# Optimization experiments

Measured on AMD Instinct MI355X. Metric: run time of the kernel, lower is better.

The kernel has to match this reference:

```python
import jax, jax.numpy as jnp
import numpy as np

B, T, I, H, CODE = 256, 512, 1, 1024, 3


def _gru_cell(x, h, Wih, Whh, bih, bhh):
    # x: [B, I], h: [B, H]; torch nn.GRU gate math
    gi = x @ Wih.T + bih            # [B, 3H]
    gh = h @ Whh.T + bhh            # [B, 3H]
    i_r, i_z, i_n = jnp.split(gi, 3, axis=-1)
    h_r, h_z, h_n = jnp.split(gh, 3, axis=-1)
    r = jax.nn.sigmoid(i_r + h_r)
    z = jax.nn.sigmoid(i_z + h_z)
    n = jnp.tanh(i_n + r * h_n)
    return (1.0 - z) * n + z * h


def setup_inputs() -> dict:
    key = jax.random.key(0)
    ks = jax.random.split(key, 16)
    s_i = 1.0 / np.sqrt(H)
    u = lambda k, shape, s: jax.random.uniform(k, shape, jnp.float32, -s, s)
    inp = {
        "input": jax.random.normal(ks[0], (B, T, I), jnp.float32),
        "hidden_state": jnp.zeros((B, H), jnp.float32),
        # encoder GRU
        "Wih_e": u(ks[1], (3 * H, I), s_i), "Whh_e": u(ks[2], (3 * H, H), s_i),
        "bih_e": u(ks[3], (3 * H,), s_i), "bhh_e": u(ks[4], (3 * H,), s_i),
        # linear_enc: H -> 3
        "Wenc": u(ks[5], (CODE, H), s_i), "benc": u(ks[6], (CODE,), s_i),
        # linear_dec: 3 -> H
        "Wdec": u(ks[7], (H, CODE), 1.0 / np.sqrt(CODE)), "bdec": u(ks[8], (H,), 1.0 / np.sqrt(CODE)),
        # decoder GRU
        "Wih_d": u(ks[9], (3 * H, I), s_i), "Whh_d": u(ks[10], (3 * H, H), s_i),
        "bih_d": u(ks[11], (3 * H,), s_i), "bhh_d": u(ks[12], (3 * H,), s_i),
        # linear_out: H -> I
        "Wout": u(ks[13], (I, H), s_i), "bout": u(ks[14], (I,), s_i),
    }
    return inp


def reference(input, hidden_state, Wih_e, Whh_e, bih_e, bhh_e,
              Wenc, benc, Wdec, bdec, Wih_d, Whh_d, bih_d, bhh_d, Wout, bout):
    # ---- Encoder: GRU over the sequence, keep final hidden state ----
    xs = jnp.swapaxes(input, 0, 1)  # [T, B, I]

    def enc_step(h, x_t):
        h = _gru_cell(x_t, h, Wih_e, Whh_e, bih_e, bhh_e)
        return h, None

    h_T, _ = jax.lax.scan(enc_step, hidden_state, xs)
    # bottleneck: linear H->3 + sigmoid (use_linear, use_activation)
    features = jax.nn.sigmoid(h_T @ Wenc.T + benc)  # [B, 3]

    h0 = features @ Wdec.T + bdec                   # [B, H]
    x0 = jnp.zeros((input.shape[0], I), input.dtype)

    def dec_step(carry, _):
        x, h = carry
        h = _gru_cell(x, h, Wih_d, Whh_d, bih_d, bhh_d)
        x = h @ Wout.T + bout                       # [B, I]
        return (x, h), x

    _, ys = jax.lax.scan(dec_step, (x0, h0), None, length=T)  # [T, B, I]
    output = jnp.swapaxes(ys, 0, 1)                 # [B, T, I]

    # ---- Masked MSE (mask is all ones in the source -> plain mean) ----
    loss = jnp.mean((input - output) ** 2)
    return loss, features, output
```

## Files before the change

kernel.cpp:

```cpp
#include <hip/hip_runtime.h>
#include <math.h>

#define B 256
#define T 512
#define H 1024
#define NBLK 256

typedef _Float16 f16x8 __attribute__((ext_vector_type(8)));
typedef float f32x4 __attribute__((ext_vector_type(4)));
typedef unsigned u32x4 __attribute__((ext_vector_type(4)));

__device__ __forceinline__ float sigmoidf_(float x) { return 1.0f / (1.0f + __expf(-x)); }
__device__ __forceinline__ float tanhf_(float x) {
    float ax = fabsf(x);
    float t = __expf(-2.0f * ax);
    float r = (1.0f - t) / (1.0f + t);
    return x < 0.f ? -r : r;
}

__device__ __forceinline__ void store_b128_coh(void* p, u32x4 v) {
    asm volatile("global_store_dwordx4 %0, %1, off sc0 sc1" :: "v"(p), "v"(v) : "memory");
}
__device__ __forceinline__ u32x4 load_b16_coh(const void* p) {
    u32x4 v;
    asm volatile("global_load_dwordx4 %0, %1, off sc0 sc1" : "=v"(v) : "v"(p));
    return v;
}
__device__ __forceinline__ void storef_coh(float* p, float v) {
    __hip_atomic_store(p, v, __ATOMIC_RELAXED, __HIP_MEMORY_SCOPE_AGENT);
}
__device__ __forceinline__ float loadf_coh(const float* p) {
    return __hip_atomic_load((float*)p, __ATOMIC_RELAXED, __HIP_MEMORY_SCOPE_AGENT);
}

__device__ __forceinline__ void load_weights(f16x8 (&wB)[48], const float* __restrict__ W,
                                             int j, int kh, int kg) {
#pragma unroll
    for (int g = 0; g < 3; ++g)
#pragma unroll
        for (int i = 0; i < 16; ++i) {
            const float* p = W + (((size_t)g << 10) + j) * 1024 + (kh << 9) + (i << 5) + (kg << 3);
            float4 u = *(const float4*)p;
            float4 v = *(const float4*)(p + 4);
            f16x8 o;
            o[0] = (_Float16)u.x; o[1] = (_Float16)u.y; o[2] = (_Float16)u.z; o[3] = (_Float16)u.w;
            o[4] = (_Float16)v.x; o[5] = (_Float16)v.y; o[6] = (_Float16)v.z; o[7] = (_Float16)v.w;
            wB[g * 16 + i] = o;
        }
}

#define PUBLISH_SYNC(hn_expr, EXTRA_STORES)                                              \
    do {                                                                                 \
        if (tid < 64) {                                                                  \
            _Float16* hn_ = (hn_expr);                                                   \
            int ch0 = tid, ch1 = tid + 64;                                               \
            store_b128_coh(hn_ + ((size_t)(b0 + (ch0 >> 3)) << 10) + j0 + (ch0 & 7) * 8, \
                           *(const u32x4*)&hout[ch0 >> 3][(ch0 & 7) * 8]);               \
            store_b128_coh(hn_ + ((size_t)(b0 + (ch1 >> 3)) << 10) + j0 + (ch1 & 7) * 8, \
                           *(const u32x4*)&hout[ch1 >> 3][(ch1 & 7) * 8]);               \
        }                                                                                \
        EXTRA_STORES                                                                     \
        if (tid >= 128 && tid < 144) {                                                   \
            unsigned tgt = gcur + 1;                                                     \
            while (__hip_atomic_load(&tags[(bt * 16 + (tid - 128)) * 32],                \
                                     __ATOMIC_RELAXED, __HIP_MEMORY_SCOPE_AGENT) < tgt)  \
                __builtin_amdgcn_s_sleep(1);                                             \
        }                                                                                \
        if (tid < 64) {                                                                  \
            asm volatile("s_waitcnt vmcnt(0)" ::: "memory");                             \
            if (tid == 0)                                                                \
                __hip_atomic_store(&tags[(bt * 16 + jt) * 32], gcur + 1,                 \
                                   __ATOMIC_RELAXED, __HIP_MEMORY_SCOPE_AGENT);          \
        }                                                                                \
        __syncthreads();                                                                 \
        ++gcur;                                                                          \
    } while (0)

template <bool DEC>
__device__ __forceinline__ void run_phase(
    int b0, int j0, int bt, int jt, int j, int np, int kh, int kg, int r16,
    int tid, int lane,
    const f16x8 (&wB)[48], float (&hreg)[4],
    _Float16* __restrict__ h16A, _Float16* __restrict__ h16B,
    const float* __restrict__ Wih, const float* __restrict__ bih,
    const float* __restrict__ bhh,
    const float* __restrict__ input, const float* __restrict__ Wout, float bout_v,
    float* __restrict__ xpart, float* __restrict__ outp,
    unsigned* tags, unsigned& gcur,
    char* Als, f32x4 (*red)[3][64], _Float16 (*hout)[64], float* xv_s, float (*xnp)[16])
{
    const float wi_r = Wih[j], wi_z = Wih[H + j], wi_n = Wih[2 * H + j];
    const float bi_r = bih[j], bi_z = bih[H + j], bi_n = bih[2 * H + j];
    const float bh_r = bhh[j], bh_z = bhh[H + j], bh_n = bhh[2 * H + j];
    const float wo = DEC ? Wout[j] : 0.f;
    const int kc = tid & 127, rb = tid >> 7;

    for (int t = 0; t < T; ++t) {
        const _Float16* hp = (t & 1) ? h16B : h16A;
        _Float16* hn = (t & 1) ? h16A : h16B;

        u32x4 tmp[4];
#pragma unroll
        for (int i = 0; i < 4; ++i) {
            int row = i * 4 + rb;
            tmp[i] = load_b16_coh(hp + ((size_t)(b0 + row) << 10) + (kc << 3));
        }
        float xg = 0.f;
        if (DEC && t > 0 && tid < 16) {
            const float* xp = xpart + ((t - 1) & 1) * 4096 + (size_t)(b0 + tid) * 16;
#pragma unroll
            for (int q = 0; q < 16; ++q) xg += loadf_coh(xp + q);
            xg += bout_v;
        }
        asm volatile("s_waitcnt vmcnt(0)" ::: "memory");
        if (DEC && tid < 16) {
            float xv = (t > 0) ? xg : 0.f;
            xv_s[tid] = xv;
            if (t > 0 && jt == 0) outp[(size_t)(b0 + tid) * T + (t - 1)] = xv;
        }
#pragma unroll
        for (int i = 0; i < 4; ++i) {
            int row = i * 4 + rb;
            *(u32x4*)(Als + row * 2048 + ((kc << 4) ^ ((row & 7) << 4))) = tmp[i];
        }
        __syncthreads();

        f32x4 aR = {0.f, 0.f, 0.f, 0.f}, aZ = {0.f, 0.f, 0.f, 0.f}, aN = {0.f, 0.f, 0.f, 0.f};
#pragma unroll
        for (int i = 0; i < 16; ++i) {
            int kb = (kh << 10) + (i << 6) + (kg << 4);
            f16x8 a = *(const f16x8*)(Als + (r16 << 11) + (kb ^ ((r16 & 7) << 4)));
            aR = __builtin_amdgcn_mfma_f32_16x16x32_f16(a, wB[i], aR, 0, 0, 0);
            aZ = __builtin_amdgcn_mfma_f32_16x16x32_f16(a, wB[16 + i], aZ, 0, 0, 0);
            aN = __builtin_amdgcn_mfma_f32_16x16x32_f16(a, wB[32 + i], aN, 0, 0, 0);
        }
        if (kh == 1) {
            red[np][0][lane] = aR; red[np][1][lane] = aZ; red[np][2][lane] = aN;
        }
        __syncthreads();

        if (kh == 0) {
            f32x4 rR = red[np][0][lane], rZ = red[np][1][lane], rN = red[np][2][lane];
#pragma unroll
            for (int reg = 0; reg < 4; ++reg) {
                int row = kg * 4 + reg;
                int b = b0 + row;
                float xv = DEC ? xv_s[row] : input[(size_t)b * T + t];
                float r = sigmoidf_(xv * wi_r + bi_r + aR[reg] + rR[reg] + bh_r);
                float z = sigmoidf_(xv * wi_z + bi_z + aZ[reg] + rZ[reg] + bh_z);
                float n = tanhf_(xv * wi_n + bi_n + r * (aN[reg] + rN[reg] + bh_n));
                float hNew = (1.f - z) * n + z * hreg[reg];
                hreg[reg] = hNew;
                hout[row][np * 16 + r16] = (_Float16)hNew;
                if (DEC) {
                    float v = hNew * wo;
                    v += __shfl_xor(v, 1); v += __shfl_xor(v, 2);
                    v += __shfl_xor(v, 4); v += __shfl_xor(v, 8);
                    if (r16 == 0) xnp[np][row] = v;
                }
            }
        }
        __syncthreads();

        PUBLISH_SYNC(hn,
            if (DEC && tid < 16) {
                float s_ = xnp[0][tid] + xnp[1][tid] + xnp[2][tid] + xnp[3][tid];
                storef_coh(xpart + (t & 1) * 4096 + (size_t)(b0 + tid) * 16 + jt, s_);
            }
        );
    }
}

__global__ __launch_bounds__(512, 2) void gru_persistent(
    const float* __restrict__ input, const float* __restrict__ h_init,
    const float* __restrict__ Wih_e, const float* __restrict__ Whh_e,
    const float* __restrict__ bih_e, const float* __restrict__ bhh_e,
    const float* __restrict__ Wenc, const float* __restrict__ benc,
    const float* __restrict__ Wdec, const float* __restrict__ bdec,
    const float* __restrict__ Wih_d, const float* __restrict__ Whh_d,
    const float* __restrict__ bih_d, const float* __restrict__ bhh_d,
    const float* __restrict__ Wout, const float* __restrict__ boutp,
    float* __restrict__ featOut, float* __restrict__ outp,
    _Float16* __restrict__ h16A, _Float16* __restrict__ h16B,
    float* __restrict__ xpart, float* __restrict__ fpart,
    unsigned* tags)
{
    __shared__ __align__(16) char Als[32768];
    __shared__ f32x4 red[4][3][64];
    __shared__ __align__(16) _Float16 hout[16][64];
    __shared__ float xv_s[16];
    __shared__ float xnp[4][16];
    __shared__ float fp_np[4][16][3];
    __shared__ float feats[16][3];

    const int tid = threadIdx.x;
    const int lane = tid & 63;
    const int wv = tid >> 6;
    const int kh = wv & 1;
    const int np = wv >> 1;
    const int kg = lane >> 4;
    const int r16 = lane & 15;
    const int bid = blockIdx.x;
    const int bt = bid & 15, jt = bid >> 4;
    const int b0 = bt * 16, j0 = jt * 64;
    const int j = j0 + np * 16 + r16;
    const float bout_v = boutp[0];
    unsigned gcur = 0;

    f16x8 wB[48];
    float hreg[4] = {0.f, 0.f, 0.f, 0.f};

    if (kh == 0) {
#pragma unroll
        for (int reg = 0; reg < 4; ++reg) {
            int row = kg * 4 + reg;
            float v = h_init[((size_t)(b0 + row) << 10) + j];
            hreg[reg] = v;
            hout[row][np * 16 + r16] = (_Float16)v;
        }
    }
    __syncthreads();
    PUBLISH_SYNC(h16A, );
    load_weights(wB, Whh_e, j, kh, kg);

    run_phase<false>(b0, j0, bt, jt, j, np, kh, kg, r16, tid, lane, wB, hreg,
                     h16A, h16B, Wih_e, bih_e, bhh_e, input, Wout, bout_v,
                     xpart, outp, tags, gcur, Als, red, hout, xv_s, xnp);

    {
        float we0 = Wenc[j], we1 = Wenc[H + j], we2 = Wenc[2 * H + j];
        if (kh == 0) {
#pragma unroll
            for (int reg = 0; reg < 4; ++reg) {
                float h = hreg[reg];
                float q0 = h * we0, q1 = h * we1, q2 = h * we2;
#pragma unroll
                for (int m = 1; m < 16; m <<= 1) {
                    q0 += __shfl_xor(q0, m);
                    q1 += __shfl_xor(q1, m);
                    q2 += __shfl_xor(q2, m);
                }
                if (r16 == 0) {
                    fp_np[np][kg * 4 + reg][0] = q0;
                    fp_np[np][kg * 4 + reg][1] = q1;
                    fp_np[np][kg * 4 + reg][2] = q2;
                }
            }
        }
        __syncthreads();
        if (tid < 48) {
            int bi = tid / 3, c = tid % 3;
            float s = fp_np[0][bi][c] + fp_np[1][bi][c] + fp_np[2][bi][c] + fp_np[3][bi][c];
            storef_coh(fpart + (size_t)(b0 + bi) * 48 + jt * 3 + c, s);
        }
        if (tid >= 128 && tid < 144) {
            unsigned tgt = gcur + 1;
            while (__hip_atomic_load(&tags[(bt * 16 + (tid - 128)) * 32],
                                     __ATOMIC_RELAXED, __HIP_MEMORY_SCOPE_AGENT) < tgt)
                __builtin_amdgcn_s_sleep(1);
        }
        if (tid < 64) {
            asm volatile("s_waitcnt vmcnt(0)" ::: "memory");
            if (tid == 0)
                __hip_atomic_store(&tags[(bt * 16 + jt) * 32], gcur + 1,
                                   __ATOMIC_RELAXED, __HIP_MEMORY_SCOPE_AGENT);
        }
        __syncthreads();
        ++gcur;

        if (tid < 48) {
            int bi = tid / 3, c = tid % 3;
            float s = 0.f;
            const float* fp = fpart + (size_t)(b0 + bi) * 48 + c;
#pragma unroll
            for (int q = 0; q < 16; ++q) s += loadf_coh(fp + q * 3);
            float f = sigmoidf_(s + benc[c]);
            feats[bi][c] = f;
            if (jt == 0) featOut[(b0 + bi) * 3 + c] = f;
        }
        __syncthreads();

        if (kh == 0) {
#pragma unroll
            for (int reg = 0; reg < 4; ++reg) {
                int row = kg * 4 + reg;
                float v = feats[row][0] * Wdec[j * 3 + 0] + feats[row][1] * Wdec[j * 3 + 1] +
                          feats[row][2] * Wdec[j * 3 + 2] + bdec[j];
                hreg[reg] = v;
                hout[row][np * 16 + r16] = (_Float16)v;
            }
        }
        __syncthreads();
        PUBLISH_SYNC(h16A, );
        load_weights(wB, Whh_d, j, kh, kg);
    }

    run_phase<true>(b0, j0, bt, jt, j, np, kh, kg, r16, tid, lane, wB, hreg,
                    h16A, h16B, Wih_d, bih_d, bhh_d, input, Wout, bout_v,
                    xpart, outp, tags, gcur, Als, red, hout, xv_s, xnp);

    if (jt == 0 && tid < 16) {
        const float* xp = xpart + 4096 + (size_t)(b0 + tid) * 16;
        float s = 0.f;
#pragma unroll
        for (int q = 0; q < 16; ++q) s += loadf_coh(xp + q);
        outp[(size_t)(b0 + tid) * T + (T - 1)] = s + bout_v;
    }
}

__global__ __launch_bounds__(256) void loss_partial(
    const float* __restrict__ input, const float* __restrict__ outp,
    float* __restrict__ partial)
{
    int idx = blockIdx.x * blockDim.x + threadIdx.x;
    float s = 0.f;
    for (int i = idx; i < B * T; i += gridDim.x * blockDim.x) {
        float d = input[i] - outp[i];
        s += d * d;
    }
#pragma unroll
    for (int off = 32; off; off >>= 1) s += __shfl_down(s, off);
    __shared__ float ws[4];
    if ((threadIdx.x & 63) == 0) ws[threadIdx.x >> 6] = s;
    __syncthreads();
    if (threadIdx.x == 0) partial[blockIdx.x] = ws[0] + ws[1] + ws[2] + ws[3];
}

__global__ __launch_bounds__(256) void loss_final(
    const float* __restrict__ partial, float* __restrict__ loss)
{
    int tid = threadIdx.x;
    float s = partial[tid];
#pragma unroll
    for (int off = 32; off; off >>= 1) s += __shfl_down(s, off);
    __shared__ float ws[4];
    if ((tid & 63) == 0) ws[tid >> 6] = s;
    __syncthreads();
    if (tid == 0) loss[0] = (ws[0] + ws[1] + ws[2] + ws[3]) * (1.0f / (float)(B * T));
}

extern "C" void kernel_launch(void* const* d_in, const int* in_sizes, int n_in,
                              void* d_out, int out_size, void* d_ws, size_t ws_size,
                              hipStream_t stream) {
    const float* input = (const float*)d_in[0];
    const float* h_init = (const float*)d_in[1];
    const float* Wih_e = (const float*)d_in[2];
    const float* Whh_e = (const float*)d_in[3];
    const float* bih_e = (const float*)d_in[4];
    const float* bhh_e = (const float*)d_in[5];
    const float* Wenc  = (const float*)d_in[6];
    const float* benc  = (const float*)d_in[7];
    const float* Wdec  = (const float*)d_in[8];
    const float* bdec  = (const float*)d_in[9];
    const float* Wih_d = (const float*)d_in[10];
    const float* Whh_d = (const float*)d_in[11];
    const float* bih_d = (const float*)d_in[12];
    const float* bhh_d = (const float*)d_in[13];
    const float* Wout  = (const float*)d_in[14];
    const float* bout  = (const float*)d_in[15];
    (void)in_sizes; (void)n_in; (void)out_size; (void)ws_size;

    float* out = (float*)d_out;
    float* lossp = out;
    float* feat = out + 1;
    float* outp = out + 1 + B * 3;

    char* ws = (char*)d_ws;
    _Float16* h16A = (_Float16*)ws;                  ws += (size_t)B * H * 2;
    _Float16* h16B = (_Float16*)ws;                  ws += (size_t)B * H * 2;
    float* xpart = (float*)ws;                       ws += 2 * 4096 * 4;
    float* fpart = (float*)ws;                       ws += (size_t)B * 48 * 4;
    float* partial = (float*)ws;                     ws += 256 * 4;
    unsigned* tags = (unsigned*)ws;                  ws += 16 * 16 * 32 * 4;

    hipMemsetAsync(tags, 0, 16 * 16 * 32 * 4, stream);

    gru_persistent<<<dim3(NBLK), dim3(512), 0, stream>>>(
        input, h_init, Wih_e, Whh_e, bih_e, bhh_e, Wenc, benc, Wdec, bdec,
        Wih_d, Whh_d, bih_d, bhh_d, Wout, bout,
        feat, outp, h16A, h16B, xpart, fpart, tags);

    loss_partial<<<256, 256, 0, stream>>>(input, outp, partial);
    loss_final<<<1, 256, 0, stream>>>(partial, lossp);
}
```

Before: 5.966 ms.

## Publish hidden state per wave with per-stripe tags instead of block barriers

Each kh==0 wave now writes its own 16-column stripe of the new hidden state and raises a per-wave tag. A single waiter wave polls all 64 stripe tags at the start of the next step, which removes the block-wide publish barrier and the extra __syncthreads at the end of every step. The decoder's output partial sums are written directly per wave into a wider xpart buffer and then reduced with vector loads and shuffles, dropping the shared xnp stage. This shortens the serial critical path of the recurrence at the cost of more tags to poll and more global partials to read.

```diff
diff --git a/kernel.cpp b/kernel.cpp
--- a/kernel.cpp
+++ b/kernel.cpp
@@ -26,11 +26,22 @@
     asm volatile("global_load_dwordx4 %0, %1, off sc0 sc1" : "=v"(v) : "v"(p));
     return v;
 }
+__device__ __forceinline__ f32x4 load_f128_coh(const void* p) {
+    f32x4 v;
+    asm volatile("global_load_dwordx4 %0, %1, off sc0 sc1" : "=v"(v) : "v"(p));
+    return v;
+}
 __device__ __forceinline__ void storef_coh(float* p, float v) {
     __hip_atomic_store(p, v, __ATOMIC_RELAXED, __HIP_MEMORY_SCOPE_AGENT);
 }
 __device__ __forceinline__ float loadf_coh(const float* p) {
     return __hip_atomic_load((float*)p, __ATOMIC_RELAXED, __HIP_MEMORY_SCOPE_AGENT);
+}
+__device__ __forceinline__ unsigned load_tag(const unsigned* p) {
+    return __hip_atomic_load((unsigned*)p, __ATOMIC_RELAXED, __HIP_MEMORY_SCOPE_AGENT);
+}
+__device__ __forceinline__ void store_tag(unsigned* p, unsigned v) {
+    __hip_atomic_store(p, v, __ATOMIC_RELAXED, __HIP_MEMORY_SCOPE_AGENT);
 }
 
 __device__ __forceinline__ void load_weights(f16x8 (&wB)[48], const float* __restrict__ W,
@@ -49,45 +60,31 @@
         }
 }
 
-#define PUBLISH_SYNC(hn_expr, EXTRA_STORES)                                              \
+#define PUBLISH_STRIPE(HN, G)                                                            \
     do {                                                                                 \
-        if (tid < 64) {                                                                  \
-            _Float16* hn_ = (hn_expr);                                                   \
-            int ch0 = tid, ch1 = tid + 64;                                               \
-            store_b128_coh(hn_ + ((size_t)(b0 + (ch0 >> 3)) << 10) + j0 + (ch0 & 7) * 8, \
-                           *(const u32x4*)&hout[ch0 >> 3][(ch0 & 7) * 8]);               \
-            store_b128_coh(hn_ + ((size_t)(b0 + (ch1 >> 3)) << 10) + j0 + (ch1 & 7) * 8, \
-                           *(const u32x4*)&hout[ch1 >> 3][(ch1 & 7) * 8]);               \
+        if (lane < 32) {                                                                 \
+            int prow = lane >> 1, pch = lane & 1;                                        \
+            u32x4 pv = *(const u32x4*)((const char*)&hout[0][0] +                        \
+                                       prow * 128 + np * 32 + pch * 16);                 \
+            store_b128_coh((HN) + ((size_t)(b0 + prow) << 10) + j0 + np * 16 + pch * 8,  \
+                           pv);                                                          \
         }                                                                                \
-        EXTRA_STORES                                                                     \
-        if (tid >= 128 && tid < 144) {                                                   \
-            unsigned tgt = gcur + 1;                                                     \
-            while (__hip_atomic_load(&tags[(bt * 16 + (tid - 128)) * 32],                \
-                                     __ATOMIC_RELAXED, __HIP_MEMORY_SCOPE_AGENT) < tgt)  \
-                __builtin_amdgcn_s_sleep(1);                                             \
-        }                                                                                \
-        if (tid < 64) {                                                                  \
-            asm volatile("s_waitcnt vmcnt(0)" ::: "memory");                             \
-            if (tid == 0)                                                                \
-                __hip_atomic_store(&tags[(bt * 16 + jt) * 32], gcur + 1,                 \
-                                   __ATOMIC_RELAXED, __HIP_MEMORY_SCOPE_AGENT);          \
-        }                                                                                \
-        __syncthreads();                                                                 \
-        ++gcur;                                                                          \
+        asm volatile("s_waitcnt vmcnt(0)" ::: "memory");                                 \
+        if (lane == 0) store_tag(gtags + (jt * 4 + np) * 16, (G));                       \
     } while (0)
 
 template <bool DEC>
 __device__ __forceinline__ void run_phase(
     int b0, int j0, int bt, int jt, int j, int np, int kh, int kg, int r16,
-    int tid, int lane,
+    int tid, int lane, int wv,
     const f16x8 (&wB)[48], float (&hreg)[4],
     _Float16* __restrict__ h16A, _Float16* __restrict__ h16B,
     const float* __restrict__ Wih, const float* __restrict__ bih,
     const float* __restrict__ bhh,
     const float* __restrict__ input, const float* __restrict__ Wout, float bout_v,
     float* __restrict__ xpart, float* __restrict__ outp,
-    unsigned* tags, unsigned& gcur,
-    char* Als, f32x4 (*red)[3][64], _Float16 (*hout)[64], float* xv_s, float (*xnp)[16])
+    unsigned* gtags, unsigned& gcur,
+    char* Als, f32x4 (*red)[3][64], _Float16 (*hout)[64], float* xv_s)
 {
     const float wi_r = Wih[j], wi_z = Wih[H + j], wi_n = Wih[2 * H + j];
     const float bi_r = bih[j], bi_z = bih[H + j], bi_n = bih[2 * H + j];
@@ -99,24 +96,40 @@
         const _Float16* hp = (t & 1) ? h16B : h16A;
         _Float16* hn = (t & 1) ? h16A : h16B;
 
+        if (wv == 1) {
+            while (load_tag(gtags + lane * 16) < gcur) __builtin_amdgcn_s_sleep(1);
+        }
+        __builtin_amdgcn_sched_barrier(0);
+        __syncthreads();
+
         u32x4 tmp[4];
 #pragma unroll
         for (int i = 0; i < 4; ++i) {
             int row = i * 4 + rb;
             tmp[i] = load_b16_coh(hp + ((size_t)(b0 + row) << 10) + (kc << 3));
         }
-        float xg = 0.f;
-        if (DEC && t > 0 && tid < 16) {
-            const float* xp = xpart + ((t - 1) & 1) * 4096 + (size_t)(b0 + tid) * 16;
-#pragma unroll
-            for (int q = 0; q < 16; ++q) xg += loadf_coh(xp + q);
-            xg += bout_v;
+        f32x4 x0 = {0.f, 0.f, 0.f, 0.f}, x1 = x0, x2 = x0, x3 = x0;
+        if (DEC && wv == 0 && t > 0) {
+            const float* xp = xpart + ((t - 1) & 1) * 16384 +
+                              (size_t)(b0 + (lane >> 2)) * 64 + (lane & 3) * 16;
+            x0 = load_f128_coh(xp);
+            x1 = load_f128_coh(xp + 4);
+            x2 = load_f128_coh(xp + 8);
+            x3 = load_f128_coh(xp + 12);
         }
         asm volatile("s_waitcnt vmcnt(0)" ::: "memory");
-        if (DEC && tid < 16) {
-            float xv = (t > 0) ? xg : 0.f;
-            xv_s[tid] = xv;
-            if (t > 0 && jt == 0) outp[(size_t)(b0 + tid) * T + (t - 1)] = xv;
+        __builtin_amdgcn_sched_barrier(0);
+        if (DEC && wv == 0) {
+            float s = x0[0] + x0[1] + x0[2] + x0[3] + x1[0] + x1[1] + x1[2] + x1[3] +
+                      x2[0] + x2[1] + x2[2] + x2[3] + x3[0] + x3[1] + x3[2] + x3[3];
+            s += __shfl_xor(s, 1);
+            s += __shfl_xor(s, 2);
+            if ((lane & 3) == 0) {
+                int row = lane >> 2;
+                float xv = (t > 0) ? (s + bout_v) : 0.f;
+                xv_s[row] = xv;
+                if (t > 0 && jt == 0) outp[(size_t)(b0 + row) * T + (t - 1)] = xv;
+            }
         }
 #pragma unroll
         for (int i = 0; i < 4; ++i) {
@@ -156,18 +169,13 @@
                     float v = hNew * wo;
                     v += __shfl_xor(v, 1); v += __shfl_xor(v, 2);
                     v += __shfl_xor(v, 4); v += __shfl_xor(v, 8);
-                    if (r16 == 0) xnp[np][row] = v;
+                    if (r16 == 0)
+                        storef_coh(xpart + (t & 1) * 16384 + (size_t)b * 64 + jt * 4 + np, v);
                 }
             }
-        }
-        __syncthreads();
-
-        PUBLISH_SYNC(hn,
-            if (DEC && tid < 16) {
-                float s_ = xnp[0][tid] + xnp[1][tid] + xnp[2][tid] + xnp[3][tid];
-                storef_coh(xpart + (t & 1) * 4096 + (size_t)(b0 + tid) * 16 + jt, s_);
-            }
-        );
+            PUBLISH_STRIPE(hn, gcur + 1);
+        }
+        ++gcur;
     }
 }
 
@@ -189,7 +197,6 @@
     __shared__ f32x4 red[4][3][64];
     __shared__ __align__(16) _Float16 hout[16][64];
     __shared__ float xv_s[16];
-    __shared__ float xnp[4][16];
     __shared__ float fp_np[4][16][3];
     __shared__ float feats[16][3];
 
@@ -205,6 +212,7 @@
     const int b0 = bt * 16, j0 = jt * 64;
     const int j = j0 + np * 16 + r16;
     const float bout_v = boutp[0];
+    unsigned* gtags = tags + (size_t)bt * 1024;
     unsigned gcur = 0;
 
     f16x8 wB[48];
@@ -218,14 +226,14 @@
             hreg[reg] = v;
             hout[row][np * 16 + r16] = (_Float16)v;
         }
-    }
-    __syncthreads();
-    PUBLISH_SYNC(h16A, );
+        PUBLISH_STRIPE(h16A, 1u);
+    }
+    gcur = 1;
     load_weights(wB, Whh_e, j, kh, kg);
 
-    run_phase<false>(b0, j0, bt, jt, j, np, kh, kg, r16, tid, lane, wB, hreg,
+    run_phase<false>(b0, j0, bt, jt, j, np, kh, kg, r16, tid, lane, wv, wB, hreg,
                      h16A, h16B, Wih_e, bih_e, bhh_e, input, Wout, bout_v,
-                     xpart, outp, tags, gcur, Als, red, hout, xv_s, xnp);
+                     xpart, outp, gtags, gcur, Als, red, hout, xv_s);
 
     {
         float we0 = Wenc[j], we1 = Wenc[H + j], we2 = Wenc[2 * H + j];
@@ -253,20 +261,15 @@
             float s = fp_np[0][bi][c] + fp_np[1][bi][c] + fp_np[2][bi][c] + fp_np[3][bi][c];
             storef_coh(fpart + (size_t)(b0 + bi) * 48 + jt * 3 + c, s);
         }
-        if (tid >= 128 && tid < 144) {
-            unsigned tgt = gcur + 1;
-            while (__hip_atomic_load(&tags[(bt * 16 + (tid - 128)) * 32],
-                                     __ATOMIC_RELAXED, __HIP_MEMORY_SCOPE_AGENT) < tgt)
-                __builtin_amdgcn_s_sleep(1);
-        }
-        if (tid < 64) {
+        if (wv == 0) {
             asm volatile("s_waitcnt vmcnt(0)" ::: "memory");
-            if (tid == 0)
-                __hip_atomic_store(&tags[(bt * 16 + jt) * 32], gcur + 1,
-                                   __ATOMIC_RELAXED, __HIP_MEMORY_SCOPE_AGENT);
-        }
-        __syncthreads();
-        ++gcur;
+            if (lane < 4) store_tag(gtags + (jt * 4 + lane) * 16, gcur + 1);
+        }
+        if (wv == 1) {
+            while (load_tag(gtags + lane * 16) < gcur + 1) __builtin_amdgcn_s_sleep(1);
+        }
+        __builtin_amdgcn_sched_barrier(0);
+        __syncthreads();
 
         if (tid < 48) {
             int bi = tid / 3, c = tid % 3;
@@ -289,22 +292,36 @@
                 hreg[reg] = v;
                 hout[row][np * 16 + r16] = (_Float16)v;
             }
-        }
-        __syncthreads();
-        PUBLISH_SYNC(h16A, );
-        load_weights(wB, Whh_d, j, kh, kg);
-    }
-
-    run_phase<true>(b0, j0, bt, jt, j, np, kh, kg, r16, tid, lane, wB, hreg,
+            PUBLISH_STRIPE(h16A, gcur + 2);
+        }
+        gcur += 2;
+    }
+    load_weights(wB, Whh_d, j, kh, kg);
+
+    run_phase<true>(b0, j0, bt, jt, j, np, kh, kg, r16, tid, lane, wv, wB, hreg,
                     h16A, h16B, Wih_d, bih_d, bhh_d, input, Wout, bout_v,
-                    xpart, outp, tags, gcur, Als, red, hout, xv_s, xnp);
-
-    if (jt == 0 && tid < 16) {
-        const float* xp = xpart + 4096 + (size_t)(b0 + tid) * 16;
-        float s = 0.f;
-#pragma unroll
-        for (int q = 0; q < 16; ++q) s += loadf_coh(xp + q);
-        outp[(size_t)(b0 + tid) * T + (T - 1)] = s + bout_v;
+                    xpart, outp, gtags, gcur, Als, red, hout, xv_s);
+
+    if (wv == 1) {
+        while (load_tag(gtags + lane * 16) < gcur) __builtin_amdgcn_s_sleep(1);
+    }
+    __builtin_amdgcn_sched_barrier(0);
+    __syncthreads();
+    if (jt == 0 && wv == 0) {
+        const float* xp = xpart + 16384 +
+                          (size_t)(b0 + (lane >> 2)) * 64 + (lane & 3) * 16;
+        f32x4 x0 = load_f128_coh(xp);
+        f32x4 x1 = load_f128_coh(xp + 4);
+        f32x4 x2 = load_f128_coh(xp + 8);
+        f32x4 x3 = load_f128_coh(xp + 12);
+        asm volatile("s_waitcnt vmcnt(0)" ::: "memory");
+        __builtin_amdgcn_sched_barrier(0);
+        float s = x0[0] + x0[1] + x0[2] + x0[3] + x1[0] + x1[1] + x1[2] + x1[3] +
+                  x2[0] + x2[1] + x2[2] + x2[3] + x3[0] + x3[1] + x3[2] + x3[3];
+        s += __shfl_xor(s, 1);
+        s += __shfl_xor(s, 2);
+        if ((lane & 3) == 0)
+            outp[(size_t)(b0 + (lane >> 2)) * T + (T - 1)] = s + bout_v;
     }
 }
 
@@ -368,12 +385,13 @@
     char* ws = (char*)d_ws;
     _Float16* h16A = (_Float16*)ws;                  ws += (size_t)B * H * 2;
     _Float16* h16B = (_Float16*)ws;                  ws += (size_t)B * H * 2;
-    float* xpart = (float*)ws;                       ws += 2 * 4096 * 4;
+    float* xpart = (float*)ws;                       ws += 2 * 16384 * 4;
     float* fpart = (float*)ws;                       ws += (size_t)B * 48 * 4;
     float* partial = (float*)ws;                     ws += 256 * 4;
-    unsigned* tags = (unsigned*)ws;                  ws += 16 * 16 * 32 * 4;
-
-    hipMemsetAsync(tags, 0, 16 * 16 * 32 * 4, stream);
+    ws = (char*)(((uintptr_t)ws + 127) & ~(uintptr_t)127);
+    unsigned* tags = (unsigned*)ws;                  ws += 16 * 1024 * 4;
+
+    hipMemsetAsync(tags, 0, 16 * 1024 * 4, stream);
 
     gru_persistent<<<dim3(NBLK), dim3(512), 0, stream>>>(
         input, h_init, Wih_e, Whh_e, bih_e, bhh_e, Wenc, benc, Wdec, bdec,
```

Result: slower. 7.197 ms (+20.6%).

## Halve persistent grid to 128 blocks of 1024 threads, widening hidden tile

Applied to the files above, without the earlier changes.

Changes the persistent GRU decomposition from 256 blocks of 512 threads (16 batch x 64 hidden columns) to 128 blocks of 1024 threads (16 batch x 128 hidden columns). Each step's global-memory barrier now spans 8 peer blocks instead of 16, which cuts polling and tag traffic, and per-block partial-sum buffers shrink to match. In exchange each block does twice the MFMA work per step, uses more shared memory, and only half the CUs are used, so per-step compute latency may grow.

```diff
diff --git a/kernel.cpp b/kernel.cpp
--- a/kernel.cpp
+++ b/kernel.cpp
@@ -4,7 +4,7 @@
 #define B 256
 #define T 512
 #define H 1024
-#define NBLK 256
+#define NBLK 128
 
 typedef _Float16 f16x8 __attribute__((ext_vector_type(8)));
 typedef float f32x4 __attribute__((ext_vector_type(4)));
@@ -53,23 +53,25 @@
     do {                                                                                 \
         if (tid < 64) {                                                                  \
             _Float16* hn_ = (hn_expr);                                                   \
-            int ch0 = tid, ch1 = tid + 64;                                               \
-            store_b128_coh(hn_ + ((size_t)(b0 + (ch0 >> 3)) << 10) + j0 + (ch0 & 7) * 8, \
-                           *(const u32x4*)&hout[ch0 >> 3][(ch0 & 7) * 8]);               \
-            store_b128_coh(hn_ + ((size_t)(b0 + (ch1 >> 3)) << 10) + j0 + (ch1 & 7) * 8, \
-                           *(const u32x4*)&hout[ch1 >> 3][(ch1 & 7) * 8]);               \
+            _Pragma("unroll")                                                            \
+            for (int pi = 0; pi < 4; ++pi) {                                             \
+                int c = tid + 64 * pi;                                                   \
+                int prow = c >> 4, pch = c & 15;                                         \
+                store_b128_coh(hn_ + ((size_t)(b0 + prow) << 10) + j0 + pch * 8,         \
+                               *(const u32x4*)&hout[prow][pch * 8]);                     \
+            }                                                                            \
         }                                                                                \
         EXTRA_STORES                                                                     \
-        if (tid >= 128 && tid < 144) {                                                   \
+        if (tid >= 128 && tid < 136) {                                                   \
             unsigned tgt = gcur + 1;                                                     \
-            while (__hip_atomic_load(&tags[(bt * 16 + (tid - 128)) * 32],                \
+            while (__hip_atomic_load(&tags[(bt * 8 + (tid - 128)) * 32],                 \
                                      __ATOMIC_RELAXED, __HIP_MEMORY_SCOPE_AGENT) < tgt)  \
                 __builtin_amdgcn_s_sleep(1);                                             \
         }                                                                                \
         if (tid < 64) {                                                                  \
             asm volatile("s_waitcnt vmcnt(0)" ::: "memory");                             \
             if (tid == 0)                                                                \
-                __hip_atomic_store(&tags[(bt * 16 + jt) * 32], gcur + 1,                 \
+                __hip_atomic_store(&tags[(bt * 8 + jt) * 32], gcur + 1,                  \
                                    __ATOMIC_RELAXED, __HIP_MEMORY_SCOPE_AGENT);          \
         }                                                                                \
         __syncthreads();                                                                 \
@@ -87,7 +89,7 @@
     const float* __restrict__ input, const float* __restrict__ Wout, float bout_v,
     float* __restrict__ xpart, float* __restrict__ outp,
     unsigned* tags, unsigned& gcur,
-    char* Als, f32x4 (*red)[3][64], _Float16 (*hout)[64], float* xv_s, float (*xnp)[16])
+    char* Als, f32x4 (*red)[3][64], _Float16 (*hout)[128], float* xv_s, float (*xnp)[16])
 {
     const float wi_r = Wih[j], wi_z = Wih[H + j], wi_n = Wih[2 * H + j];
     const float bi_r = bih[j], bi_z = bih[H + j], bi_n = bih[2 * H + j];
@@ -99,30 +101,24 @@
         const _Float16* hp = (t & 1) ? h16B : h16A;
         _Float16* hn = (t & 1) ? h16A : h16B;
 
-        u32x4 tmp[4];
-#pragma unroll
-        for (int i = 0; i < 4; ++i) {
-            int row = i * 4 + rb;
-            tmp[i] = load_b16_coh(hp + ((size_t)(b0 + row) << 10) + (kc << 3));
-        }
+        u32x4 tmp0 = load_b16_coh(hp + ((size_t)(b0 + rb) << 10) + (kc << 3));
+        u32x4 tmp1 = load_b16_coh(hp + ((size_t)(b0 + rb + 8) << 10) + (kc << 3));
         float xg = 0.f;
         if (DEC && t > 0 && tid < 16) {
-            const float* xp = xpart + ((t - 1) & 1) * 4096 + (size_t)(b0 + tid) * 16;
-#pragma unroll
-            for (int q = 0; q < 16; ++q) xg += loadf_coh(xp + q);
+            const float* xp = xpart + ((t - 1) & 1) * 2048 + (size_t)(b0 + tid) * 8;
+#pragma unroll
+            for (int q = 0; q < 8; ++q) xg += loadf_coh(xp + q);
             xg += bout_v;
         }
         asm volatile("s_waitcnt vmcnt(0)" ::: "memory");
+        __builtin_amdgcn_sched_barrier(0);
         if (DEC && tid < 16) {
             float xv = (t > 0) ? xg : 0.f;
             xv_s[tid] = xv;
             if (t > 0 && jt == 0) outp[(size_t)(b0 + tid) * T + (t - 1)] = xv;
         }
-#pragma unroll
-        for (int i = 0; i < 4; ++i) {
-            int row = i * 4 + rb;
-            *(u32x4*)(Als + row * 2048 + ((kc << 4) ^ ((row & 7) << 4))) = tmp[i];
-        }
+        *(u32x4*)(Als + rb * 2048 + ((kc << 4) ^ ((rb & 7) << 4))) = tmp0;
+        *(u32x4*)(Als + (rb + 8) * 2048 + ((kc << 4) ^ ((rb & 7) << 4))) = tmp1;
         __syncthreads();
 
         f32x4 aR = {0.f, 0.f, 0.f, 0.f}, aZ = {0.f, 0.f, 0.f, 0.f}, aN = {0.f, 0.f, 0.f, 0.f};
@@ -164,14 +160,15 @@
 
         PUBLISH_SYNC(hn,
             if (DEC && tid < 16) {
-                float s_ = xnp[0][tid] + xnp[1][tid] + xnp[2][tid] + xnp[3][tid];
-                storef_coh(xpart + (t & 1) * 4096 + (size_t)(b0 + tid) * 16 + jt, s_);
+                float s_ = xnp[0][tid] + xnp[1][tid] + xnp[2][tid] + xnp[3][tid] +
+                           xnp[4][tid] + xnp[5][tid] + xnp[6][tid] + xnp[7][tid];
+                storef_coh(xpart + (t & 1) * 2048 + (size_t)(b0 + tid) * 8 + jt, s_);
             }
         );
     }
 }
 
-__global__ __launch_bounds__(512, 2) void gru_persistent(
+__global__ __launch_bounds__(1024) void gru_persistent(
     const float* __restrict__ input, const float* __restrict__ h_init,
     const float* __restrict__ Wih_e, const float* __restrict__ Whh_e,
     const float* __restrict__ bih_e, const float* __restrict__ bhh_e,
@@ -186,11 +183,11 @@
     unsigned* tags)
 {
     __shared__ __align__(16) char Als[32768];
-    __shared__ f32x4 red[4][3][64];
-    __shared__ __align__(16) _Float16 hout[16][64];
+    __shared__ f32x4 red[8][3][64];
+    __shared__ __align__(16) _Float16 hout[16][128];
     __shared__ float xv_s[16];
-    __shared__ float xnp[4][16];
-    __shared__ float fp_np[4][16][3];
+    __shared__ float xnp[8][16];
+    __shared__ float fp_np[8][16][3];
     __shared__ float feats[16][3];
 
     const int tid = threadIdx.x;
@@ -202,7 +199,7 @@
     const int r16 = lane & 15;
     const int bid = blockIdx.x;
     const int bt = bid & 15, jt = bid >> 4;
-    const int b0 = bt * 16, j0 = jt * 64;
+    const int b0 = bt * 16, j0 = jt * 128;
     const int j = j0 + np * 16 + r16;
     const float bout_v = boutp[0];
     unsigned gcur = 0;
@@ -250,19 +247,21 @@
         __syncthreads();
         if (tid < 48) {
             int bi = tid / 3, c = tid % 3;
-            float s = fp_np[0][bi][c] + fp_np[1][bi][c] + fp_np[2][bi][c] + fp_np[3][bi][c];
-            storef_coh(fpart + (size_t)(b0 + bi) * 48 + jt * 3 + c, s);
-        }
-        if (tid >= 128 && tid < 144) {
+            float s = 0.f;
+#pragma unroll
+            for (int q = 0; q < 8; ++q) s += fp_np[q][bi][c];
+            storef_coh(fpart + (size_t)(b0 + bi) * 24 + jt * 3 + c, s);
+        }
+        if (tid >= 128 && tid < 136) {
             unsigned tgt = gcur + 1;
-            while (__hip_atomic_load(&tags[(bt * 16 + (tid - 128)) * 32],
+            while (__hip_atomic_load(&tags[(bt * 8 + (tid - 128)) * 32],
                                      __ATOMIC_RELAXED, __HIP_MEMORY_SCOPE_AGENT) < tgt)
                 __builtin_amdgcn_s_sleep(1);
         }
         if (tid < 64) {
             asm volatile("s_waitcnt vmcnt(0)" ::: "memory");
             if (tid == 0)
-                __hip_atomic_store(&tags[(bt * 16 + jt) * 32], gcur + 1,
+                __hip_atomic_store(&tags[(bt * 8 + jt) * 32], gcur + 1,
                                    __ATOMIC_RELAXED, __HIP_MEMORY_SCOPE_AGENT);
         }
         __syncthreads();
@@ -271,9 +270,9 @@
         if (tid < 48) {
             int bi = tid / 3, c = tid % 3;
             float s = 0.f;
-            const float* fp = fpart + (size_t)(b0 + bi) * 48 + c;
-#pragma unroll
-            for (int q = 0; q < 16; ++q) s += loadf_coh(fp + q * 3);
+            const float* fp = fpart + (size_t)(b0 + bi) * 24 + c;
+#pragma unroll
+            for (int q = 0; q < 8; ++q) s += loadf_coh(fp + q * 3);
             float f = sigmoidf_(s + benc[c]);
             feats[bi][c] = f;
             if (jt == 0) featOut[(b0 + bi) * 3 + c] = f;
@@ -300,10 +299,10 @@
                     xpart, outp, tags, gcur, Als, red, hout, xv_s, xnp);
 
     if (jt == 0 && tid < 16) {
-        const float* xp = xpart + 4096 + (size_t)(b0 + tid) * 16;
+        const float* xp = xpart + 2048 + (size_t)(b0 + tid) * 8;
         float s = 0.f;
 #pragma unroll
-        for (int q = 0; q < 16; ++q) s += loadf_coh(xp + q);
+        for (int q = 0; q < 8; ++q) s += loadf_coh(xp + q);
         outp[(size_t)(b0 + tid) * T + (T - 1)] = s + bout_v;
     }
 }
@@ -368,14 +367,15 @@
     char* ws = (char*)d_ws;
     _Float16* h16A = (_Float16*)ws;                  ws += (size_t)B * H * 2;
     _Float16* h16B = (_Float16*)ws;                  ws += (size_t)B * H * 2;
-    float* xpart = (float*)ws;                       ws += 2 * 4096 * 4;
-    float* fpart = (float*)ws;                       ws += (size_t)B * 48 * 4;
+    float* xpart = (float*)ws;                       ws += 2 * 2048 * 4;
+    float* fpart = (float*)ws;                       ws += (size_t)B * 24 * 4;
     float* partial = (float*)ws;                     ws += 256 * 4;
-    unsigned* tags = (unsigned*)ws;                  ws += 16 * 16 * 32 * 4;
-
-    hipMemsetAsync(tags, 0, 16 * 16 * 32 * 4, stream);
-
-    gru_persistent<<<dim3(NBLK), dim3(512), 0, stream>>>(
+    ws = (char*)(((uintptr_t)ws + 127) & ~(uintptr_t)127);
+    unsigned* tags = (unsigned*)ws;                  ws += 16 * 8 * 32 * 4;
+
+    hipMemsetAsync(tags, 0, 16 * 8 * 32 * 4, stream);
+
+    gru_persistent<<<dim3(NBLK), dim3(1024), 0, stream>>>(
         input, h_init, Wih_e, Whh_e, bih_e, bhh_e, Wenc, benc, Wdec, bdec,
         Wih_d, Whh_d, bih_d, bhh_d, Wout, bout,
         feat, outp, h16A, h16B, xpart, fpart, tags);
```

Result: slower. 20.78 ms (+248.3%).
